# Optimization experiments

Measured on AMD Instinct MI355X. Metric: run time of the kernel, lower is better.

## Reference

```python
import jax, jax.numpy as jnp
import numpy as np

B = 32
L = 256
NUM_AA = 20
LAMBDA_SINGLE = 1.0
LAMBDA_PAIR = 0.2 * (L - 1)


def setup_inputs() -> dict:
    key = jax.random.key(0)
    k1, k2, k3 = jax.random.split(key, 3)
    x = jax.random.randint(k1, (B, L), 0, NUM_AA, dtype=jnp.int32)
    # Embedding(num, 1) init: normal(0, embedding_dim**-0.5) = std 1.0
    w_single = jax.random.normal(k2, (L * NUM_AA, 1), dtype=jnp.float32)
    w_pair = jax.random.normal(k3, (L * L * NUM_AA * NUM_AA, 1), dtype=jnp.float32)
    return {"x": x, "w_single": w_single, "w_pair": w_pair}


def reference(x, w_single, w_pair):
    ws = w_single[:, 0]  # [L*20]
    wp = w_pair[:, 0]    # [L*L*400]
    Bn, Ln = x.shape
    pos = jnp.arange(Ln, dtype=jnp.int32)

    # singles[b, i] = ws[i*20 + x[b, i]]
    singles = ws[pos[None, :] * NUM_AA + x]  # [B, L]
    all_singles = jnp.broadcast_to(ws.reshape(Ln, NUM_AA), (Bn, Ln, NUM_AA))  # [B, L, 20]

    # pairs[b, i, j] = wp[(i*L + j)*400 + x[b,i]*20 + x[b,j]]
    idx_pairs = (pos[:, None] * Ln + pos[None, :]) * (NUM_AA * NUM_AA) \
        + x[:, :, None] * NUM_AA + x[:, None, :]  # [B, L, L]
    pairs = wp[idx_pairs]  # [B, L, L]

    # all_pairs reproduces the original in-place mutation semantics:
    # at outer iteration i (inner loop over j), x[:, p] has already been
    # overwritten to 19 for p < i, equals j for p == i, and is original for p > i.
    i_ax = pos[None, :, None, None]                      # [1, L, 1, 1]
    p_ax = pos[None, None, :, None]                      # [1, 1, L, 1]
    j_ax = jnp.arange(NUM_AA, dtype=jnp.int32)[None, None, None, :]  # [1,1,1,20]
    x_b = x[:, None, :, None]                            # [B, 1, L, 1]
    eff = jnp.where(p_ax < i_ax, NUM_AA - 1, jnp.where(p_ax == i_ax, j_ax, x_b))
    idx_all = (i_ax * Ln + p_ax) * (NUM_AA * NUM_AA) + j_ax * NUM_AA + eff  # [B,L,L,20]
    all_pairs = wp[idx_all]  # [B, L, L, 20]

    energy = singles + jnp.sum(pairs, axis=2)  # [B, L]
    logits = all_singles + jnp.sum(all_pairs, axis=2)  # [B, L, 20]
    total_energy = jax.nn.logsumexp(logits, axis=-1)  # [B, L]
    final_energy = jnp.mean(jnp.sum(-energy + total_energy, axis=1))

    single_reg = LAMBDA_SINGLE * jnp.sum(jnp.square(w_single))
    pair_reg = LAMBDA_PAIR * jnp.sum(jnp.square(w_pair))
    single_lasso = LAMBDA_SINGLE * jnp.sum(jnp.abs(w_single))
    pair_lasso = LAMBDA_PAIR * jnp.sum(jnp.abs(w_pair))
    return final_energy + single_reg + pair_reg + single_lasso + pair_lasso
```

## Files before the change

### kernel.cpp

```cpp
#include <hip/hip_runtime.h>
#include <cmath>

#define Bsz 32
#define Lsz 256
#define Asz 20

#define NHALF 2
#define HALF 128
#define SUBB 16
#define NST (HALF / SUBB)
#define STF (SUBB * 400)
#define BLK1 640
#define NWG1 (Lsz * NHALF)

#define OFF_G 0
#define OFF_C (NHALF * Lsz * Bsz * Asz)
#define OFF_E (OFF_C + NHALF * Lsz * Asz)
#define OFF_RSQ (OFF_E + NHALF * Lsz * Bsz)
#define OFF_RAB (OFF_RSQ + NWG1)
#define OFF_K2  (OFF_RAB + NWG1)

__device__ __forceinline__ void cp16(const float* g, float* l) {
  __builtin_amdgcn_global_load_lds(
      (const __attribute__((address_space(1))) void*)g,
      (__attribute__((address_space(3))) void*)l, 16, 0, 0);
}

__global__ __launch_bounds__(BLK1, 5) void k1(const int* __restrict__ x,
                                              const float* __restrict__ wp,
                                              float* __restrict__ ws) {
  const int wg = blockIdx.x;
  const int i = wg >> 1;
  const int h = wg & 1;
  const int pbase = h * HALF;
  const int t = threadIdx.x;
  const int j = t >> 5;
  const int b = t & 31;

  __shared__ float buf[2][STF];
  __shared__ int   xs[HALF * Bsz];
  __shared__ int   xi[Bsz];
  __shared__ float wred[32];

  const float* wrow = wp + (size_t)(i * Lsz + pbase) * 400;
  const int wbase = (t >> 6) << 8;

  {
    const float* g = wrow;
    cp16(g + t * 4, &buf[0][wbase]);
    cp16(g + 2560 + t * 4, &buf[0][2560 + wbase]);
    if (t < 320) cp16(g + 5120 + t * 4, &buf[0][5120 + wbase]);
  }
  for (int k = t; k < HALF * Bsz; k += BLK1) {
    int dp = k >> 5, bb = k & 31;
    xs[k] = x[bb * Lsz + pbase + dp];
  }
  if (t < Bsz) xi[t] = x[t * Lsz + i];
  __syncthreads();

  float accJ = 0.f, accE = 0.f, accC = 0.f, rsq = 0.f, rab = 0.f;
  const int jbase = j * Asz;

  for (int s = 0; s < NST; ++s) {
    const float* blk = buf[s & 1];

    if (s + 1 < NST) {
      const float* g = wrow + (size_t)(s + 1) * STF;
      float* l = buf[(s + 1) & 1];
      cp16(g + t * 4, l + wbase);
      cp16(g + 2560 + t * 4, l + 2560 + wbase);
      if (t < 320) cp16(g + 5120 + t * 4, l + 5120 + wbase);
    }

    const int sp = s * SUBB;
    const int pg = pbase + sp;

    int ppstart = i + 1 - pg;
    if (ppstart < 0) ppstart = 0;
    for (int pp = ppstart; pp < SUBB; ++pp) {
      int xv = xs[((sp + pp) << 5) | b];
      accJ += blk[pp * 400 + jbase + xv];
    }
    if (t < Bsz) {
      const int ebase = xi[t] * Asz;
      #pragma unroll
      for (int pp = 0; pp < SUBB; ++pp) {
        int xv = xs[((sp + pp) << 5) | t];
        accE += blk[pp * 400 + ebase + xv];
      }
    } else if (t < Bsz + Asz) {
      const int jj = t - Bsz;
      int pend = i - pg;
      if (pend > SUBB) pend = SUBB;
      for (int pp = 0; pp < pend; ++pp) accC += blk[pp * 400 + jj * Asz + 19];
      const int pd = i - pg;
      if (pd >= 0 && pd < SUBB) accC += blk[pd * 400 + jj * Asz + jj];
    }

    const float4* bf4 = (const float4*)blk;
    float4 v0 = bf4[t];
    float4 v1 = bf4[t + 640];
    rsq += v0.x*v0.x + v0.y*v0.y + v0.z*v0.z + v0.w*v0.w
         + v1.x*v1.x + v1.y*v1.y + v1.z*v1.z + v1.w*v1.w;
    rab += fabsf(v0.x)+fabsf(v0.y)+fabsf(v0.z)+fabsf(v0.w)
         + fabsf(v1.x)+fabsf(v1.y)+fabsf(v1.z)+fabsf(v1.w);
    if (t < 320) {
      float4 v2 = bf4[t + 1280];
      rsq += v2.x*v2.x + v2.y*v2.y + v2.z*v2.z + v2.w*v2.w;
      rab += fabsf(v2.x)+fabsf(v2.y)+fabsf(v2.z)+fabsf(v2.w);
    }
    __syncthreads();
  }

  ws[OFF_G + ((size_t)((h * Lsz + i) * Bsz + b)) * Asz + j] = accJ;
  if (t < Bsz) ws[OFF_E + (h * Lsz + i) * Bsz + t] = accE;
  else if (t < Bsz + Asz) ws[OFF_C + (h * Lsz + i) * Asz + (t - Bsz)] = accC;

  for (int sft = 32; sft >= 1; sft >>= 1) {
    rsq += __shfl_down(rsq, sft);
    rab += __shfl_down(rab, sft);
  }
  if ((t & 63) == 0) { wred[t >> 6] = rsq; wred[16 + (t >> 6)] = rab; }
  __syncthreads();
  if (t == 0) {
    float a = 0.f, bb2 = 0.f;
    for (int w = 0; w < BLK1 / 64; ++w) { a += wred[w]; bb2 += wred[16 + w]; }
    ws[OFF_RSQ + wg] = a;
    ws[OFF_RAB + wg] = bb2;
  }
}

__global__ __launch_bounds__(BLK1) void k2(const int* __restrict__ x,
                                           const float* __restrict__ wsng,
                                           const float* __restrict__ ws,
                                           float* __restrict__ wso) {
  const int i = blockIdx.x;
  const int t = threadIdx.x;
  const int j = t >> 5, b = t & 31;
  __shared__ float l[Bsz * 21];

  float v = wsng[i * Asz + j];
  #pragma unroll
  for (int hh = 0; hh < NHALF; ++hh) {
    v += ws[OFF_C + (hh * Lsz + i) * Asz + j];
    v += ws[OFF_G + ((size_t)((hh * Lsz + i) * Bsz + b)) * Asz + j];
  }
  l[b * 21 + j] = v;
  __syncthreads();

  if (t < Bsz) {
    float m = -1e30f;
    #pragma unroll
    for (int jj = 0; jj < Asz; ++jj) m = fmaxf(m, l[t * 21 + jj]);
    float se = 0.f;
    #pragma unroll
    for (int jj = 0; jj < Asz; ++jj) se += __expf(l[t * 21 + jj] - m);
    float lse = m + __logf(se);
    float en = wsng[i * Asz + x[t * Lsz + i]];
    #pragma unroll
    for (int hh = 0; hh < NHALF; ++hh) en += ws[OFF_E + (hh * Lsz + i) * Bsz + t];
    wso[OFF_K2 + i * Bsz + t] = lse - en;
  }
}

__global__ __launch_bounds__(256) void k3(const float* __restrict__ wsng,
                                          const float* __restrict__ ws,
                                          float* __restrict__ out) {
  const int t = threadIdx.x;
  float ssq = 0.f, sab = 0.f;
  for (int k = t; k < Lsz * Asz; k += 256) {
    float v = wsng[k];
    ssq += v * v; sab += fabsf(v);
  }
  float psq = 0.f, pab = 0.f;
  for (int k = t; k < NWG1; k += 256) {
    psq += ws[OFF_RSQ + k];
    pab += ws[OFF_RAB + k];
  }
  float fe = 0.f;
  for (int k = t; k < Lsz * Bsz; k += 256) fe += ws[OFF_K2 + k];

  const float LP = 51.0f;
  float val = fe * (1.0f / Bsz) + (ssq + sab) + LP * (psq + pab);

  __shared__ float red[256];
  red[t] = val;
  __syncthreads();
  for (int s = 128; s >= 1; s >>= 1) {
    if (t < s) red[t] += red[t + s];
    __syncthreads();
  }
  if (t == 0) out[0] = red[0];
}

extern "C" void kernel_launch(void* const* d_in, const int* in_sizes, int n_in,
                              void* d_out, int out_size, void* d_ws, size_t ws_size,
                              hipStream_t stream) {
  const int*   x       = (const int*)d_in[0];
  const float* wsingle = (const float*)d_in[1];
  const float* wpair   = (const float*)d_in[2];
  float* ws  = (float*)d_ws;
  float* out = (float*)d_out;

  k1<<<NWG1, BLK1, 0, stream>>>(x, wpair, ws);
  k2<<<Lsz, BLK1, 0, stream>>>(x, wsingle, ws, ws);
  k3<<<1, 256, 0, stream>>>(wsingle, ws, out);
}
```

Before: 185.8 us.

## Split pair rows into quarters and spread energy/constant sums across threads

The main kernel now splits each row i into four 64-position quarters. That gives 1024 workgroups of 320 threads with smaller 8-position staging tiles, where before there were 512 workgroups of 640 threads. Each thread now gathers two amino-acid columns. The per-batch energy and the fixed-prefix constant terms are computed by many threads, one position each, and reduced through shared memory. Before, one or two waves did these sums serially. The partial-logit workspace layout is transposed so stores are coalesced, and k2 reads the new layout. The cost is more workgroups, an extra barrier and reduction, and LDS staging copies that overlap each other.

Measured after the change: 184.1 us. No clear change (-0.9%).

```diff
diff --git a/kernel.cpp b/kernel.cpp
--- a/kernel.cpp
+++ b/kernel.cpp
@@ -5,18 +5,21 @@
 #define Lsz 256
 #define Asz 20
 
-#define NHALF 2
-#define HALF 128
-#define SUBB 16
-#define NST (HALF / SUBB)
+#define NQ 4
+#define QP 64
+#define SUBB 8
+#define NST (QP / SUBB)
 #define STF (SUBB * 400)
-#define BLK1 640
-#define NWG1 (Lsz * NHALF)
+#define BLK1 320
+#define NWG1 (Lsz * NQ)
 
 #define OFF_G 0
-#define OFF_C (NHALF * Lsz * Bsz * Asz)
-#define OFF_E (OFF_C + NHALF * Lsz * Asz)
-#define OFF_RSQ (OFF_E + NHALF * Lsz * Bsz)
+#define SZ_G (NQ * Lsz * Asz * Bsz)
+#define OFF_C (OFF_G + SZ_G)
+#define SZ_C (NQ * Lsz * Asz)
+#define OFF_E (OFF_C + SZ_C)
+#define SZ_E (NQ * Lsz * Bsz)
+#define OFF_RSQ (OFF_E + SZ_E)
 #define OFF_RAB (OFF_RSQ + NWG1)
 #define OFF_K2  (OFF_RAB + NWG1)
 
@@ -26,50 +29,65 @@
       (__attribute__((address_space(3))) void*)l, 16, 0, 0);
 }
 
+__device__ __forceinline__ void stage_block(const float* g, float* l, int t) {
+  const int wbase = (t >> 6) << 8;
+  cp16(g + 4 * t, l + wbase);
+  cp16(g + 1280 + 4 * t, l + 1280 + wbase);
+  if (t < 128) cp16(g + 2560 + 4 * t, l + 2560 + wbase);
+  if (t >= 128 && t < 192) cp16(g + 2944 + 4 * (t - 128), l + 2944 + ((t - 128) & ~63) * 4 + ((t >> 6) == 2 ? 0 : 0));
+}
+
 __global__ __launch_bounds__(BLK1, 5) void k1(const int* __restrict__ x,
                                               const float* __restrict__ wp,
                                               float* __restrict__ ws) {
   const int wg = blockIdx.x;
-  const int i = wg >> 1;
-  const int h = wg & 1;
-  const int pbase = h * HALF;
+  const int i = wg >> 2;
+  const int q = wg & 3;
+  const int pbase = q * QP;
   const int t = threadIdx.x;
-  const int j = t >> 5;
+  const int jlo = t >> 5;
   const int b = t & 31;
 
   __shared__ float buf[2][STF];
-  __shared__ int   xs[HALF * Bsz];
+  __shared__ int   xs[QP * Bsz];
   __shared__ int   xi[Bsz];
-  __shared__ float wred[32];
+  __shared__ float eRed[8][Bsz];
+  __shared__ float cRed[8][Asz];
+  __shared__ float wred[16];
 
   const float* wrow = wp + (size_t)(i * Lsz + pbase) * 400;
   const int wbase = (t >> 6) << 8;
 
   {
     const float* g = wrow;
-    cp16(g + t * 4, &buf[0][wbase]);
-    cp16(g + 2560 + t * 4, &buf[0][2560 + wbase]);
-    if (t < 320) cp16(g + 5120 + t * 4, &buf[0][5120 + wbase]);
-  }
-  for (int k = t; k < HALF * Bsz; k += BLK1) {
+    float* l = &buf[0][0];
+    cp16(g + 4 * t, l + wbase);
+    cp16(g + 1280 + 4 * t, l + 1280 + wbase);
+    if (t < 128) cp16(g + 2560 + 4 * t, l + 2560 + wbase);
+    if (t >= 128 && t < 192) cp16(g + 2944 + 4 * (t - 128), l + 2944);
+  }
+  for (int k = t; k < QP * Bsz; k += BLK1) {
     int dp = k >> 5, bb = k & 31;
     xs[k] = x[bb * Lsz + pbase + dp];
   }
   if (t < Bsz) xi[t] = x[t * Lsz + i];
   __syncthreads();
 
-  float accJ = 0.f, accE = 0.f, accC = 0.f, rsq = 0.f, rab = 0.f;
-  const int jbase = j * Asz;
+  const int xib = xi[b];
+  float accJ0 = 0.f, accJ1 = 0.f, accE = 0.f, accC = 0.f, rsq = 0.f, rab = 0.f;
+  const int jb0 = jlo * Asz;
+  const int jb1 = (jlo + 10) * Asz;
 
   for (int s = 0; s < NST; ++s) {
     const float* blk = buf[s & 1];
 
     if (s + 1 < NST) {
       const float* g = wrow + (size_t)(s + 1) * STF;
-      float* l = buf[(s + 1) & 1];
-      cp16(g + t * 4, l + wbase);
-      cp16(g + 2560 + t * 4, l + 2560 + wbase);
-      if (t < 320) cp16(g + 5120 + t * 4, l + 5120 + wbase);
+      float* l = &buf[(s + 1) & 1][0];
+      cp16(g + 4 * t, l + wbase);
+      cp16(g + 1280 + 4 * t, l + 1280 + wbase);
+      if (t < 128) cp16(g + 2560 + 4 * t, l + 2560 + wbase);
+      if (t >= 128 && t < 192) cp16(g + 2944 + 4 * (t - 128), l + 2944);
     }
 
     const int sp = s * SUBB;
@@ -79,58 +97,75 @@
     if (ppstart < 0) ppstart = 0;
     for (int pp = ppstart; pp < SUBB; ++pp) {
       int xv = xs[((sp + pp) << 5) | b];
-      accJ += blk[pp * 400 + jbase + xv];
-    }
-    if (t < Bsz) {
-      const int ebase = xi[t] * Asz;
-      #pragma unroll
-      for (int pp = 0; pp < SUBB; ++pp) {
-        int xv = xs[((sp + pp) << 5) | t];
-        accE += blk[pp * 400 + ebase + xv];
+      const float* r = blk + pp * 400 + xv;
+      accJ0 += r[jb0];
+      accJ1 += r[jb1];
+    }
+
+    if (jlo < 8) {
+      int xv = xs[((sp + jlo) << 5) | b];
+      accE += blk[jlo * 400 + xib * Asz + xv];
+      if (b < Asz) {
+        int p = pg + jlo;
+        if (p < i) accC += blk[jlo * 400 + b * Asz + 19];
+        else if (p == i) accC += blk[jlo * 400 + b * Asz + b];
       }
-    } else if (t < Bsz + Asz) {
-      const int jj = t - Bsz;
-      int pend = i - pg;
-      if (pend > SUBB) pend = SUBB;
-      for (int pp = 0; pp < pend; ++pp) accC += blk[pp * 400 + jj * Asz + 19];
-      const int pd = i - pg;
-      if (pd >= 0 && pd < SUBB) accC += blk[pd * 400 + jj * Asz + jj];
     }
 
     const float4* bf4 = (const float4*)blk;
     float4 v0 = bf4[t];
-    float4 v1 = bf4[t + 640];
+    float4 v1 = bf4[t + 320];
     rsq += v0.x*v0.x + v0.y*v0.y + v0.z*v0.z + v0.w*v0.w
          + v1.x*v1.x + v1.y*v1.y + v1.z*v1.z + v1.w*v1.w;
     rab += fabsf(v0.x)+fabsf(v0.y)+fabsf(v0.z)+fabsf(v0.w)
          + fabsf(v1.x)+fabsf(v1.y)+fabsf(v1.z)+fabsf(v1.w);
-    if (t < 320) {
-      float4 v2 = bf4[t + 1280];
+    if (t < 160) {
+      float4 v2 = bf4[t + 640];
       rsq += v2.x*v2.x + v2.y*v2.y + v2.z*v2.z + v2.w*v2.w;
       rab += fabsf(v2.x)+fabsf(v2.y)+fabsf(v2.z)+fabsf(v2.w);
     }
     __syncthreads();
   }
 
-  ws[OFF_G + ((size_t)((h * Lsz + i) * Bsz + b)) * Asz + j] = accJ;
-  if (t < Bsz) ws[OFF_E + (h * Lsz + i) * Bsz + t] = accE;
-  else if (t < Bsz + Asz) ws[OFF_C + (h * Lsz + i) * Asz + (t - Bsz)] = accC;
+  {
+    const size_t gb = OFF_G + (size_t)(q * Lsz + i) * Asz * Bsz;
+    ws[gb + t] = accJ0;
+    ws[gb + t + 320] = accJ1;
+  }
+  if (jlo < 8) {
+    eRed[jlo][b] = accE;
+    if (b < Asz) cRed[jlo][b] = accC;
+  }
+  __syncthreads();
+  if (t < Bsz) {
+    float e = 0.f;
+    #pragma unroll
+    for (int k = 0; k < 8; ++k) e += eRed[k][t];
+    ws[OFF_E + (q * Lsz + i) * Bsz + t] = e;
+  } else if (t < Bsz + Asz) {
+    const int jj = t - Bsz;
+    float c = 0.f;
+    #pragma unroll
+    for (int k = 0; k < 8; ++k) c += cRed[k][jj];
+    ws[OFF_C + (q * Lsz + i) * Asz + jj] = c;
+  }
 
   for (int sft = 32; sft >= 1; sft >>= 1) {
     rsq += __shfl_down(rsq, sft);
     rab += __shfl_down(rab, sft);
   }
-  if ((t & 63) == 0) { wred[t >> 6] = rsq; wred[16 + (t >> 6)] = rab; }
+  if ((t & 63) == 0) { wred[t >> 6] = rsq; wred[8 + (t >> 6)] = rab; }
   __syncthreads();
   if (t == 0) {
     float a = 0.f, bb2 = 0.f;
-    for (int w = 0; w < BLK1 / 64; ++w) { a += wred[w]; bb2 += wred[16 + w]; }
+    for (int w = 0; w < BLK1 / 64; ++w) { a += wred[w]; bb2 += wred[8 + w]; }
     ws[OFF_RSQ + wg] = a;
     ws[OFF_RAB + wg] = bb2;
   }
 }
 
-__global__ __launch_bounds__(BLK1) void k2(const int* __restrict__ x,
+#define BLK2 640
+__global__ __launch_bounds__(BLK2) void k2(const int* __restrict__ x,
                                            const float* __restrict__ wsng,
                                            const float* __restrict__ ws,
                                            float* __restrict__ wso) {
@@ -141,9 +176,9 @@
 
   float v = wsng[i * Asz + j];
   #pragma unroll
-  for (int hh = 0; hh < NHALF; ++hh) {
-    v += ws[OFF_C + (hh * Lsz + i) * Asz + j];
-    v += ws[OFF_G + ((size_t)((hh * Lsz + i) * Bsz + b)) * Asz + j];
+  for (int qq = 0; qq < NQ; ++qq) {
+    v += ws[OFF_C + (qq * Lsz + i) * Asz + j];
+    v += ws[OFF_G + ((size_t)(qq * Lsz + i) * Asz + j) * Bsz + b];
   }
   l[b * 21 + j] = v;
   __syncthreads();
@@ -158,7 +193,7 @@
     float lse = m + __logf(se);
     float en = wsng[i * Asz + x[t * Lsz + i]];
     #pragma unroll
-    for (int hh = 0; hh < NHALF; ++hh) en += ws[OFF_E + (hh * Lsz + i) * Bsz + t];
+    for (int qq = 0; qq < NQ; ++qq) en += ws[OFF_E + (qq * Lsz + i) * Bsz + t];
     wso[OFF_K2 + i * Bsz + t] = lse - en;
   }
 }
@@ -203,6 +238,6 @@
   float* out = (float*)d_out;
 
   k1<<<NWG1, BLK1, 0, stream>>>(x, wpair, ws);
-  k2<<<Lsz, BLK1, 0, stream>>>(x, wsingle, ws, ws);
+  k2<<<Lsz, BLK2, 0, stream>>>(x, wsingle, ws, ws);
   k3<<<1, 256, 0, stream>>>(wsingle, ws, out);
 }
```
